# Optimization experiments

Hardware: AMD Instinct MI355X
Metric: run time of the kernel (lower is better)

Reference implementation:

```python
import jax, jax.numpy as jnp
import numpy as np

N, D, K = 65536, 512, 5


def setup_inputs() -> dict:
    key = jax.random.key(0)
    k0, k1, k2, k3, k4 = jax.random.split(key, 5)
    x = jax.random.normal(k0, (N, D), dtype=jnp.float32)
    is_protected = jax.random.randint(k1, (N,), 0, 2) > 0  # bool mask
    alpha_p = jax.random.uniform(k2, (D,), dtype=jnp.float32, minval=0.9, maxval=1.1)
    classif_w = jax.random.normal(k3, (K, 1), dtype=jnp.float32)
    centroids = jax.random.normal(k4, (K, D), dtype=jnp.float32)
    return {"x": x, "is_protected": is_protected, "alpha_p": alpha_p,
            "classif_w": classif_w, "centroids": centroids}


def reference(x, is_protected, alpha_p, classif_w, centroids):
    # NOTE: original torch forward applies alpha_p to both the protected and
    # non-protected rows (alpha_np is unused), so the mask split is a no-op
    # and we compute the mapping over all rows at once.
    # distances: sum_d alpha_d * (x_nd - c_kd)^2  -> (n, k)
    diff2 = (x[:, None, :] - centroids[None, :, :]) ** 2  # (n, k, d)
    dist = jnp.einsum("nkd,d->nk", diff2, alpha_p)
    mapping = jax.nn.softmax(dist, axis=-1)              # (n, k)
    reconstructed = mapping @ centroids                  # (n, d)
    pred = (mapping @ jax.nn.sigmoid(classif_w)).ravel() # (n,)
    return mapping, reconstructed, pred
```

## Files before the change

### kernel.cpp

```cpp
#include <hip/hip_runtime.h>
#include <math.h>

#define LFR_N 65536
#define LFR_D 512
#define LFR_K 5
#define ROWS  4

typedef float fx4 __attribute__((ext_vector_type(4)));

__global__ __launch_bounds__(256) void lfr_kernel(
    const float* __restrict__ x,
    const float* __restrict__ alpha,
    const float* __restrict__ w,
    const float* __restrict__ cent,
    float* __restrict__ out_map,
    float* __restrict__ out_rec,
    float* __restrict__ out_pred)
{
    const int lane          = threadIdx.x & 63;
    const int wave_in_block = threadIdx.x >> 6;
    const int wave_id       = blockIdx.x * (blockDim.x >> 6) + wave_in_block;
    const int rb            = wave_id * ROWS;
    if (rb >= LFR_N) return;

    const int d0  = lane * 8;
    const int hi  = (lane >> 5) & 1;
    const int mid = (lane >> 4) & 1;

    float4 xl[ROWS][2];
    #pragma unroll
    for (int r = 0; r < ROWS; ++r) {
        const float* xr = x + (size_t)(rb + r) * LFR_D + d0;
        xl[r][0] = *(const float4*)(xr);
        xl[r][1] = *(const float4*)(xr + 4);
    }

    float al[8];
    {
        float4 a0 = *(const float4*)(alpha + d0);
        float4 a1 = *(const float4*)(alpha + d0 + 4);
        al[0]=a0.x; al[1]=a0.y; al[2]=a0.z; al[3]=a0.w;
        al[4]=a1.x; al[5]=a1.y; al[6]=a1.z; al[7]=a1.w;
    }
    float c[LFR_K][8];
    #pragma unroll
    for (int k = 0; k < LFR_K; ++k) {
        float4 c0 = *(const float4*)(cent + k * LFR_D + d0);
        float4 c1 = *(const float4*)(cent + k * LFR_D + d0 + 4);
        c[k][0]=c0.x; c[k][1]=c0.y; c[k][2]=c0.z; c[k][3]=c0.w;
        c[k][4]=c1.x; c[k][5]=c1.y; c[k][6]=c1.z; c[k][7]=c1.w;
    }
    float m2a[8];
    #pragma unroll
    for (int j = 0; j < 8; ++j) m2a[j] = -2.0f * al[j];
    float cst[LFR_K];
    #pragma unroll
    for (int k = 0; k < LFR_K; ++k) {
        float s = 0.0f;
        #pragma unroll
        for (int j = 0; j < 8; ++j) {
            float u = al[j] * c[k][j];
            s = fmaf(u, c[k][j], s);
        }
        cst[k] = s;
    }

    float xv[ROWS][8];
    #pragma unroll
    for (int r = 0; r < ROWS; ++r) {
        xv[r][0]=xl[r][0].x; xv[r][1]=xl[r][0].y; xv[r][2]=xl[r][0].z; xv[r][3]=xl[r][0].w;
        xv[r][4]=xl[r][1].x; xv[r][5]=xl[r][1].y; xv[r][6]=xl[r][1].z; xv[r][7]=xl[r][1].w;
    }
    float p[ROWS][LFR_K];
    #pragma unroll
    for (int r = 0; r < ROWS; ++r) {
        float v[8];
        #pragma unroll
        for (int j = 0; j < 8; ++j) v[j] = m2a[j] * xv[r][j];
        #pragma unroll
        for (int k = 0; k < LFR_K; ++k) {
            float acc = cst[k];
            #pragma unroll
            for (int j = 0; j < 8; ++j) acc = fmaf(c[k][j], v[j], acc);
            p[r][k] = acc;
        }
    }

    float q[2][LFR_K];
    #pragma unroll
    for (int r2 = 0; r2 < 2; ++r2) {
        #pragma unroll
        for (int k = 0; k < LFR_K; ++k) {
            float send = hi ? p[r2][k]     : p[2 + r2][k];
            float keep = hi ? p[2 + r2][k] : p[r2][k];
            q[r2][k] = keep + __shfl_xor(send, 32);
        }
    }
    float s[LFR_K];
    #pragma unroll
    for (int k = 0; k < LFR_K; ++k) {
        float send = mid ? q[0][k] : q[1][k];
        float keep = mid ? q[1][k] : q[0][k];
        s[k] = keep + __shfl_xor(send, 16);
    }
    #pragma unroll
    for (int off = 8; off > 0; off >>= 1) {
        #pragma unroll
        for (int k = 0; k < LFR_K; ++k)
            s[k] += __shfl_xor(s[k], off);
    }

    float e[LFR_K];
    {
        float mx = s[0];
        #pragma unroll
        for (int k = 1; k < LFR_K; ++k) mx = fmaxf(mx, s[k]);
        float sum = 0.0f;
        #pragma unroll
        for (int k = 0; k < LFR_K; ++k) { e[k] = __expf(s[k] - mx); sum += e[k]; }
        float inv = 1.0f / sum;
        #pragma unroll
        for (int k = 0; k < LFR_K; ++k) e[k] *= inv;
    }

    if ((lane & 15) == 0) {
        const int g = lane >> 4;
        float sigw[LFR_K];
        #pragma unroll
        for (int k = 0; k < LFR_K; ++k)
            sigw[k] = 1.0f / (1.0f + __expf(-w[k]));
        float* mp = out_map + (size_t)(rb + g) * LFR_K;
        *(float4*)(mp) = make_float4(e[0], e[1], e[2], e[3]);
        mp[4] = e[4];
        float pr = e[0] * sigw[0];
        #pragma unroll
        for (int k = 1; k < LFR_K; ++k) pr = fmaf(e[k], sigw[k], pr);
        out_pred[rb + g] = pr;
    }

    float mA[2][LFR_K];
    #pragma unroll
    for (int k = 0; k < LFR_K; ++k) {
        float o = __shfl_xor(e[k], 16);
        mA[0][k] = mid ? o    : e[k];
        mA[1][k] = mid ? e[k] : o;
    }
    float M[ROWS][LFR_K];
    #pragma unroll
    for (int r2 = 0; r2 < 2; ++r2) {
        #pragma unroll
        for (int k = 0; k < LFR_K; ++k) {
            float o = __shfl_xor(mA[r2][k], 32);
            M[r2][k]     = hi ? o         : mA[r2][k];
            M[2 + r2][k] = hi ? mA[r2][k] : o;
        }
    }

    #pragma unroll
    for (int r = 0; r < ROWS; ++r) {
        float rv[8];
        #pragma unroll
        for (int j = 0; j < 8; ++j) {
            float acc = M[r][0] * c[0][j];
            #pragma unroll
            for (int k = 1; k < LFR_K; ++k) acc = fmaf(M[r][k], c[k][j], acc);
            rv[j] = acc;
        }
        float* rr = out_rec + (size_t)(rb + r) * LFR_D + d0;
        fx4 v0 = { rv[0], rv[1], rv[2], rv[3] };
        fx4 v1 = { rv[4], rv[5], rv[6], rv[7] };
        __builtin_nontemporal_store(v0, (fx4*)(rr));
        __builtin_nontemporal_store(v1, (fx4*)(rr + 4));
    }
}

extern "C" void kernel_launch(void* const* d_in, const int* in_sizes, int n_in,
                              void* d_out, int out_size, void* d_ws, size_t ws_size,
                              hipStream_t stream) {
    const float* x     = (const float*)d_in[0];
    const float* alpha = (const float*)d_in[2];
    const float* w     = (const float*)d_in[3];
    const float* cent  = (const float*)d_in[4];

    float* out   = (float*)d_out;
    float* o_map = out;
    float* o_rec = out + (size_t)LFR_N * LFR_K;
    float* o_prd = out + (size_t)LFR_N * LFR_K + (size_t)LFR_N * LFR_D;

    dim3 grid(LFR_N / (4 * ROWS)), block(256);
    lfr_kernel<<<grid, block, 0, stream>>>(x, alpha, w, cent, o_map, o_rec, o_prd);
}
```

Baseline: 244.4 us.

## Use persistent grid-stride waves with register prefetch of next rows

Launches a fixed grid of 1024 blocks, with each wave looping over 4 iterations of 4 rows. Per-wave setup (alpha, centroid loads, constants, sigmoid of weights) is amortized across iterations, and the next iteration's x rows are prefetched into registers during the current compute. It also replaces the nontemporal stores of the reconstruction with plain float4 stores. The costs are higher register pressure from the prefetch and possibly more cache pollution from the normal stores.

```diff
diff --git a/kernel.cpp b/kernel.cpp
--- a/kernel.cpp
+++ b/kernel.cpp
@@ -4,9 +4,10 @@
 #define LFR_N 65536
 #define LFR_D 512
 #define LFR_K 5
-#define ROWS  4
-
-typedef float fx4 __attribute__((ext_vector_type(4)));
+#define ROWS   4
+#define BLOCKS 1024
+#define NWAVES (BLOCKS * 4)
+#define ITERS  (LFR_N / (NWAVES * ROWS))
 
 __global__ __launch_bounds__(256) void lfr_kernel(
     const float* __restrict__ x,
@@ -17,23 +18,13 @@
     float* __restrict__ out_rec,
     float* __restrict__ out_pred)
 {
-    const int lane          = threadIdx.x & 63;
-    const int wave_in_block = threadIdx.x >> 6;
-    const int wave_id       = blockIdx.x * (blockDim.x >> 6) + wave_in_block;
-    const int rb            = wave_id * ROWS;
-    if (rb >= LFR_N) return;
+    const int lane = threadIdx.x & 63;
+    const int wib  = threadIdx.x >> 6;
+    const int wid  = blockIdx.x * (blockDim.x >> 6) + wib;
 
     const int d0  = lane * 8;
     const int hi  = (lane >> 5) & 1;
     const int mid = (lane >> 4) & 1;
-
-    float4 xl[ROWS][2];
-    #pragma unroll
-    for (int r = 0; r < ROWS; ++r) {
-        const float* xr = x + (size_t)(rb + r) * LFR_D + d0;
-        xl[r][0] = *(const float4*)(xr);
-        xl[r][1] = *(const float4*)(xr + 4);
-    }
 
     float al[8];
     {
@@ -64,113 +55,128 @@
         }
         cst[k] = s;
     }
+    float sigw[LFR_K];
+    #pragma unroll
+    for (int k = 0; k < LFR_K; ++k)
+        sigw[k] = 1.0f / (1.0f + __expf(-w[k]));
 
-    float xv[ROWS][8];
+    const size_t XSTEP = (size_t)NWAVES * ROWS * LFR_D;
+    const float* xp = x + (size_t)wid * ROWS * LFR_D + d0;
+
+    float4 xl[ROWS][2];
     #pragma unroll
     for (int r = 0; r < ROWS; ++r) {
-        xv[r][0]=xl[r][0].x; xv[r][1]=xl[r][0].y; xv[r][2]=xl[r][0].z; xv[r][3]=xl[r][0].w;
-        xv[r][4]=xl[r][1].x; xv[r][5]=xl[r][1].y; xv[r][6]=xl[r][1].z; xv[r][7]=xl[r][1].w;
+        xl[r][0] = *(const float4*)(xp + (size_t)r * LFR_D);
+        xl[r][1] = *(const float4*)(xp + (size_t)r * LFR_D + 4);
     }
-    float p[ROWS][LFR_K];
-    #pragma unroll
-    for (int r = 0; r < ROWS; ++r) {
-        float v[8];
+
+    for (int it = 0; it < ITERS; ++it) {
+        const size_t rbase = (size_t)(it * NWAVES + wid) * ROWS;
+
+        float p[ROWS][LFR_K];
         #pragma unroll
-        for (int j = 0; j < 8; ++j) v[j] = m2a[j] * xv[r][j];
+        for (int r = 0; r < ROWS; ++r) {
+            float v[8];
+            v[0]=m2a[0]*xl[r][0].x; v[1]=m2a[1]*xl[r][0].y;
+            v[2]=m2a[2]*xl[r][0].z; v[3]=m2a[3]*xl[r][0].w;
+            v[4]=m2a[4]*xl[r][1].x; v[5]=m2a[5]*xl[r][1].y;
+            v[6]=m2a[6]*xl[r][1].z; v[7]=m2a[7]*xl[r][1].w;
+            #pragma unroll
+            for (int k = 0; k < LFR_K; ++k) {
+                float acc = cst[k];
+                #pragma unroll
+                for (int j = 0; j < 8; ++j) acc = fmaf(c[k][j], v[j], acc);
+                p[r][k] = acc;
+            }
+            if (it + 1 < ITERS) {
+                const float* nx = xp + XSTEP + (size_t)r * LFR_D;
+                xl[r][0] = *(const float4*)(nx);
+                xl[r][1] = *(const float4*)(nx + 4);
+            }
+        }
+
+        float q[2][LFR_K];
+        #pragma unroll
+        for (int r2 = 0; r2 < 2; ++r2) {
+            #pragma unroll
+            for (int k = 0; k < LFR_K; ++k) {
+                float send = hi ? p[r2][k]     : p[2 + r2][k];
+                float keep = hi ? p[2 + r2][k] : p[r2][k];
+                q[r2][k] = keep + __shfl_xor(send, 32);
+            }
+        }
+        float s[LFR_K];
         #pragma unroll
         for (int k = 0; k < LFR_K; ++k) {
-            float acc = cst[k];
+            float send = mid ? q[0][k] : q[1][k];
+            float keep = mid ? q[1][k] : q[0][k];
+            s[k] = keep + __shfl_xor(send, 16);
+        }
+        #pragma unroll
+        for (int off = 8; off > 0; off >>= 1) {
             #pragma unroll
-            for (int j = 0; j < 8; ++j) acc = fmaf(c[k][j], v[j], acc);
-            p[r][k] = acc;
+            for (int k = 0; k < LFR_K; ++k)
+                s[k] += __shfl_xor(s[k], off);
         }
-    }
 
-    float q[2][LFR_K];
-    #pragma unroll
-    for (int r2 = 0; r2 < 2; ++r2) {
+        float e[LFR_K];
+        {
+            float mx = s[0];
+            #pragma unroll
+            for (int k = 1; k < LFR_K; ++k) mx = fmaxf(mx, s[k]);
+            float sum = 0.0f;
+            #pragma unroll
+            for (int k = 0; k < LFR_K; ++k) { e[k] = __expf(s[k] - mx); sum += e[k]; }
+            float inv = 1.0f / sum;
+            #pragma unroll
+            for (int k = 0; k < LFR_K; ++k) e[k] *= inv;
+        }
+
+        if ((lane & 15) == 0) {
+            const int g = lane >> 4;
+            float* mp = out_map + (rbase + g) * LFR_K;
+            *(float4*)(mp) = make_float4(e[0], e[1], e[2], e[3]);
+            mp[4] = e[4];
+            float pr = e[0] * sigw[0];
+            #pragma unroll
+            for (int k = 1; k < LFR_K; ++k) pr = fmaf(e[k], sigw[k], pr);
+            out_pred[rbase + g] = pr;
+        }
+
+        float mA[2][LFR_K];
         #pragma unroll
         for (int k = 0; k < LFR_K; ++k) {
-            float send = hi ? p[r2][k]     : p[2 + r2][k];
-            float keep = hi ? p[2 + r2][k] : p[r2][k];
-            q[r2][k] = keep + __shfl_xor(send, 32);
+            float o = __shfl_xor(e[k], 16);
+            mA[0][k] = mid ? o    : e[k];
+            mA[1][k] = mid ? e[k] : o;
         }
-    }
-    float s[LFR_K];
-    #pragma unroll
-    for (int k = 0; k < LFR_K; ++k) {
-        float send = mid ? q[0][k] : q[1][k];
-        float keep = mid ? q[1][k] : q[0][k];
-        s[k] = keep + __shfl_xor(send, 16);
-    }
-    #pragma unroll
-    for (int off = 8; off > 0; off >>= 1) {
+        float M[ROWS][LFR_K];
         #pragma unroll
-        for (int k = 0; k < LFR_K; ++k)
-            s[k] += __shfl_xor(s[k], off);
-    }
+        for (int r2 = 0; r2 < 2; ++r2) {
+            #pragma unroll
+            for (int k = 0; k < LFR_K; ++k) {
+                float o = __shfl_xor(mA[r2][k], 32);
+                M[r2][k]     = hi ? o         : mA[r2][k];
+                M[2 + r2][k] = hi ? mA[r2][k] : o;
+            }
+        }
 
-    float e[LFR_K];
-    {
-        float mx = s[0];
         #pragma unroll
-        for (int k = 1; k < LFR_K; ++k) mx = fmaxf(mx, s[k]);
-        float sum = 0.0f;
-        #pragma unroll
-        for (int k = 0; k < LFR_K; ++k) { e[k] = __expf(s[k] - mx); sum += e[k]; }
-        float inv = 1.0f / sum;
-        #pragma unroll
-        for (int k = 0; k < LFR_K; ++k) e[k] *= inv;
-    }
+        for (int r = 0; r < ROWS; ++r) {
+            float rv[8];
+            #pragma unroll
+            for (int j = 0; j < 8; ++j) {
+                float acc = M[r][0] * c[0][j];
+                #pragma unroll
+                for (int k = 1; k < LFR_K; ++k) acc = fmaf(M[r][k], c[k][j], acc);
+                rv[j] = acc;
+            }
+            float* rr = out_rec + (rbase + r) * LFR_D + d0;
+            *(float4*)(rr)     = make_float4(rv[0], rv[1], rv[2], rv[3]);
+            *(float4*)(rr + 4) = make_float4(rv[4], rv[5], rv[6], rv[7]);
+        }
 
-    if ((lane & 15) == 0) {
-        const int g = lane >> 4;
-        float sigw[LFR_K];
-        #pragma unroll
-        for (int k = 0; k < LFR_K; ++k)
-            sigw[k] = 1.0f / (1.0f + __expf(-w[k]));
-        float* mp = out_map + (size_t)(rb + g) * LFR_K;
-        *(float4*)(mp) = make_float4(e[0], e[1], e[2], e[3]);
-        mp[4] = e[4];
-        float pr = e[0] * sigw[0];
-        #pragma unroll
-        for (int k = 1; k < LFR_K; ++k) pr = fmaf(e[k], sigw[k], pr);
-        out_pred[rb + g] = pr;
-    }
-
-    float mA[2][LFR_K];
-    #pragma unroll
-    for (int k = 0; k < LFR_K; ++k) {
-        float o = __shfl_xor(e[k], 16);
-        mA[0][k] = mid ? o    : e[k];
-        mA[1][k] = mid ? e[k] : o;
-    }
-    float M[ROWS][LFR_K];
-    #pragma unroll
-    for (int r2 = 0; r2 < 2; ++r2) {
-        #pragma unroll
-        for (int k = 0; k < LFR_K; ++k) {
-            float o = __shfl_xor(mA[r2][k], 32);
-            M[r2][k]     = hi ? o         : mA[r2][k];
-            M[2 + r2][k] = hi ? mA[r2][k] : o;
-        }
-    }
-
-    #pragma unroll
-    for (int r = 0; r < ROWS; ++r) {
-        float rv[8];
-        #pragma unroll
-        for (int j = 0; j < 8; ++j) {
-            float acc = M[r][0] * c[0][j];
-            #pragma unroll
-            for (int k = 1; k < LFR_K; ++k) acc = fmaf(M[r][k], c[k][j], acc);
-            rv[j] = acc;
-        }
-        float* rr = out_rec + (size_t)(rb + r) * LFR_D + d0;
-        fx4 v0 = { rv[0], rv[1], rv[2], rv[3] };
-        fx4 v1 = { rv[4], rv[5], rv[6], rv[7] };
-        __builtin_nontemporal_store(v0, (fx4*)(rr));
-        __builtin_nontemporal_store(v1, (fx4*)(rr + 4));
+        xp += XSTEP;
     }
 }
 
@@ -187,6 +193,6 @@
     float* o_rec = out + (size_t)LFR_N * LFR_K;
     float* o_prd = out + (size_t)LFR_N * LFR_K + (size_t)LFR_N * LFR_D;
 
-    dim3 grid(LFR_N / (4 * ROWS)), block(256);
+    dim3 grid(BLOCKS), block(256);
     lfr_kernel<<<grid, block, 0, stream>>>(x, alpha, w, cent, o_map, o_rec, o_prd);
 }
```

Result: no change. 246.5 us (+0.9%).
